# Performance work log

Measured on AMD Instinct MI355X. Metric: run time of the kernel, lower is better.

Reference implementation:

```python
import jax, jax.numpy as jnp
import numpy as np

STRIDE = (16, 16)
PADDING = (0, 0)


def setup_inputs() -> dict:
    key = jax.random.key(0)
    k1, k2, k3 = jax.random.split(key, 3)
    x = jax.random.normal(k1, (16, 12, 512, 512), dtype=jnp.float32)
    weight = jax.random.normal(k2, (768, 1, 16, 16), dtype=jnp.float32) * 0.02
    bias = jax.random.normal(k3, (768,), dtype=jnp.float32) * 0.02
    return {"x": x, "weight": weight, "bias": bias}


def reference(x, weight, bias):
    # Faithful to the torch module: groups=c conv with the shared filter
    # repeated per input channel, then mean over the channel axis, then bias.
    b, c, h, w = x.shape
    o = weight.shape[0]
    # groups=c conv with repeated weight == independent conv of each channel
    # with the same (o,1,kh,kw) filter; fold channels into batch.
    xc = x.reshape(b * c, 1, h, w)
    y = jax.lax.conv_general_dilated(
        xc, weight,
        window_strides=STRIDE,
        padding=[(PADDING[0], PADDING[0]), (PADDING[1], PADDING[1])],
        dimension_numbers=("NCHW", "OIHW", "NCHW"),
    )  # (b*c, o, H', W')
    hp, wp = y.shape[-2], y.shape[-1]
    y = y.reshape(b, c, o, hp, wp).mean(axis=1)  # (b, o, H', W')
    y = y + bias[None, :, None, None]
    return y
```

## Files before the change

### kernel.cpp

```cpp
#include <hip/hip_runtime.h>
#include <hip/hip_bf16.h>

#define BATCH 16
#define CIN   12
#define HIMG  512
#define WIMG  512
#define OCH   768
#define KDIM  256
#define HW    (HIMG*WIMG)
#define NPATCH 1024

#define MEAN_BLOCKS 4096
#define PACK_BLOCKS 96

typedef __attribute__((ext_vector_type(8))) short short8;
typedef __attribute__((ext_vector_type(4))) float f32x4;

__global__ __launch_bounds__(256) void mean_pack_kernel(
        const float* __restrict__ x, __hip_bfloat16* __restrict__ xm,
        const float* __restrict__ w, short8* __restrict__ wbp) {
    const int bid = blockIdx.x;
    if (bid < MEAN_BLOCKS) {
        int idx = bid * 256 + threadIdx.x;
        int b = idx >> 16;
        int pos = (idx & 65535) << 2;
        const float* px = x + (size_t)b * CIN * HW + pos;
        float sx = 0.f, sy = 0.f, sz = 0.f, sw = 0.f;
        #pragma unroll
        for (int c = 0; c < CIN; ++c) {
            f32x4 v = *reinterpret_cast<const f32x4*>(px + (size_t)c * HW);
            sx += v.x; sy += v.y; sz += v.z; sw += v.w;
        }
        const float inv = 1.0f / 12.0f;
        union { ushort4 u4; __hip_bfloat16 h[4]; } o;
        o.h[0] = __float2bfloat16(sx * inv);
        o.h[1] = __float2bfloat16(sy * inv);
        o.h[2] = __float2bfloat16(sz * inv);
        o.h[3] = __float2bfloat16(sw * inv);
        *reinterpret_cast<ushort4*>(xm + (size_t)idx * 4) = o.u4;
    } else {
        int u = (bid - MEAN_BLOCKS) * 256 + threadIdx.x;
        int lane = u & 63;
        int kk   = (u >> 6) & 7;
        int ot   = u >> 9;
        int o = ot * 16 + (lane & 15);
        int k = kk * 32 + (lane >> 4) * 8;
        const float* src = w + (size_t)o * KDIM + k;
        f32x4 v0 = *reinterpret_cast<const f32x4*>(src);
        f32x4 v1 = *reinterpret_cast<const f32x4*>(src + 4);
        union { short8 s; __hip_bfloat16 h[8]; } t;
        t.h[0] = __float2bfloat16(v0.x);
        t.h[1] = __float2bfloat16(v0.y);
        t.h[2] = __float2bfloat16(v0.z);
        t.h[3] = __float2bfloat16(v0.w);
        t.h[4] = __float2bfloat16(v1.x);
        t.h[5] = __float2bfloat16(v1.y);
        t.h[6] = __float2bfloat16(v1.z);
        t.h[7] = __float2bfloat16(v1.w);
        wbp[u] = t.s;
    }
}

#define LDB 264

__global__ __launch_bounds__(512, 4) void gemm_kernel(
        const short8* __restrict__ wbp,
        const __hip_bfloat16* __restrict__ xm,
        const float* __restrict__ bias,
        float* __restrict__ out) {
    __shared__ short Bl[32][LDB];

    const int tid = threadIdx.x;
    const int b  = blockIdx.x >> 5;
    const int is = blockIdx.x & 31;

    {
        const int r = tid >> 5;
        const int j = tid & 31;
        const short* src = reinterpret_cast<const short*>(
            xm + (size_t)b * HW + (size_t)(is * 16 + r) * WIMG + j * 16);
        *reinterpret_cast<short8*>(&Bl[j][r * 16])     = *reinterpret_cast<const short8*>(src);
        *reinterpret_cast<short8*>(&Bl[j][r * 16 + 8]) = *reinterpret_cast<const short8*>(src + 8);
    }
    __syncthreads();

    const int lane = tid & 63;
    const int wv   = tid >> 6;
    const int lrow = lane & 15;
    const int lg   = lane >> 4;

    f32x4 acc[6][2] = {};
    const short8* wp = wbp + (size_t)(wv * 6) * 8 * 64 + lane;

    #pragma unroll
    for (int kk = 0; kk < 8; ++kk) {
        short8 af[6], bf[2];
        #pragma unroll
        for (int fo = 0; fo < 6; ++fo)
            af[fo] = wp[(size_t)(fo * 8 + kk) * 64];
        #pragma unroll
        for (int fm = 0; fm < 2; ++fm)
            bf[fm] = *reinterpret_cast<const short8*>(&Bl[fm * 16 + lrow][kk * 32 + lg * 8]);
        #pragma unroll
        for (int fo = 0; fo < 6; ++fo)
            #pragma unroll
            for (int fm = 0; fm < 2; ++fm)
                acc[fo][fm] = __builtin_amdgcn_mfma_f32_16x16x32_bf16(af[fo], bf[fm], acc[fo][fm], 0, 0, 0);
    }

    const int p0 = is * 32;
    float* ob = out + (size_t)b * OCH * NPATCH + p0;
    #pragma unroll
    for (int fo = 0; fo < 6; ++fo) {
        const int obase = wv * 96 + fo * 16 + lg * 4;
        #pragma unroll
        for (int r = 0; r < 4; ++r) {
            const int o = obase + r;
            const float bv = bias[o];
            float* orow = ob + (size_t)o * NPATCH;
            #pragma unroll
            for (int fm = 0; fm < 2; ++fm)
                orow[fm * 16 + lrow] = acc[fo][fm][r] + bv;
        }
    }
}

extern "C" void kernel_launch(void* const* d_in, const int* in_sizes, int n_in,
                              void* d_out, int out_size, void* d_ws, size_t ws_size,
                              hipStream_t stream) {
    const float* x    = (const float*)d_in[0];
    const float* w    = (const float*)d_in[1];
    const float* bias = (const float*)d_in[2];
    float* out = (float*)d_out;

    __hip_bfloat16* xm = (__hip_bfloat16*)d_ws;
    short8* wbp = (short8*)((char*)d_ws + (size_t)BATCH * HW * 2);

    mean_pack_kernel<<<MEAN_BLOCKS + PACK_BLOCKS, 256, 0, stream>>>(x, xm, w, wbp);
    gemm_kernel<<<BATCH * 32, 512, 0, stream>>>(wbp, xm, bias, out);
}
```

Measured before the change: 54.23 us.

## Retile GEMM blocks to 128 patches by 192 output channels

Each GEMM block previously covered 32 patches and all 768 output channels. It now covers a 128-patch tile (four patch rows) and a quarter of the output channels, with the 8 waves arranged as 2 output-channel groups by 4 patch groups. This cuts per-block weight fetch from L2 and spreads work differently across the 512 blocks. The cost is a 4x larger LDS footprint per block (about 67KB), which may reduce occupancy, and each patch tile is now loaded by four blocks.

After: 57.18 us. +5.4%, slower.

```diff
diff --git a/kernel.cpp b/kernel.cpp
--- a/kernel.cpp
+++ b/kernel.cpp
@@ -68,29 +68,40 @@
         const __hip_bfloat16* __restrict__ xm,
         const float* __restrict__ bias,
         float* __restrict__ out) {
-    __shared__ short Bl[32][LDB];
+    __shared__ short Bl[128][LDB];
 
     const int tid = threadIdx.x;
-    const int b  = blockIdx.x >> 5;
-    const int is = blockIdx.x & 31;
+    const int mt = blockIdx.x >> 2;
+    const int ot = blockIdx.x & 3;
+    const int b  = mt >> 3;
+    const int sq = mt & 7;
 
     {
-        const int r = tid >> 5;
-        const int j = tid & 31;
-        const short* src = reinterpret_cast<const short*>(
-            xm + (size_t)b * HW + (size_t)(is * 16 + r) * WIMG + j * 16);
-        *reinterpret_cast<short8*>(&Bl[j][r * 16])     = *reinterpret_cast<const short8*>(src);
-        *reinterpret_cast<short8*>(&Bl[j][r * 16 + 8]) = *reinterpret_cast<const short8*>(src + 8);
+        const __hip_bfloat16* xb = xm + (size_t)b * HW + (size_t)(sq * 64) * WIMG;
+        #pragma unroll
+        for (int it = 0; it < 8; ++it) {
+            const int g   = it * 512 + tid;
+            const int r   = g >> 6;
+            const int c   = g & 63;
+            const int si  = r >> 4;
+            const int r16 = r & 15;
+            *reinterpret_cast<short8*>(
+                &Bl[si * 32 + (c >> 1)][r16 * 16 + (c & 1) * 8]) =
+                *reinterpret_cast<const short8*>(
+                    reinterpret_cast<const short*>(xb + (size_t)r * WIMG) + c * 8);
+        }
     }
     __syncthreads();
 
     const int lane = tid & 63;
     const int wv   = tid >> 6;
+    const int wo   = wv >> 2;
+    const int wm   = wv & 3;
     const int lrow = lane & 15;
     const int lg   = lane >> 4;
 
     f32x4 acc[6][2] = {};
-    const short8* wp = wbp + (size_t)(wv * 6) * 8 * 64 + lane;
+    const short8* wp = wbp + (size_t)(ot * 12 + wo * 6) * 8 * 64 + lane;
 
     #pragma unroll
     for (int kk = 0; kk < 8; ++kk) {
@@ -100,7 +111,8 @@
             af[fo] = wp[(size_t)(fo * 8 + kk) * 64];
         #pragma unroll
         for (int fm = 0; fm < 2; ++fm)
-            bf[fm] = *reinterpret_cast<const short8*>(&Bl[fm * 16 + lrow][kk * 32 + lg * 8]);
+            bf[fm] = *reinterpret_cast<const short8*>(
+                &Bl[wm * 32 + fm * 16 + lrow][kk * 32 + lg * 8]);
         #pragma unroll
         for (int fo = 0; fo < 6; ++fo)
             #pragma unroll
@@ -108,11 +120,10 @@
                 acc[fo][fm] = __builtin_amdgcn_mfma_f32_16x16x32_bf16(af[fo], bf[fm], acc[fo][fm], 0, 0, 0);
     }
 
-    const int p0 = is * 32;
-    float* ob = out + (size_t)b * OCH * NPATCH + p0;
+    float* ob = out + (size_t)b * OCH * NPATCH + sq * 128 + wm * 32;
     #pragma unroll
     for (int fo = 0; fo < 6; ++fo) {
-        const int obase = wv * 96 + fo * 16 + lg * 4;
+        const int obase = ot * 192 + wo * 96 + fo * 16 + lg * 4;
         #pragma unroll
         for (int r = 0; r < 4; ++r) {
             const int o = obase + r;
@@ -137,5 +148,5 @@
     short8* wbp = (short8*)((char*)d_ws + (size_t)BATCH * HW * 2);
 
     mean_pack_kernel<<<MEAN_BLOCKS + PACK_BLOCKS, 256, 0, stream>>>(x, xm, w, wbp);
-    gemm_kernel<<<BATCH * 32, 512, 0, stream>>>(wbp, xm, bias, out);
+    gemm_kernel<<<512, 512, 0, stream>>>(wbp, xm, bias, out);
 }
```
